# Kernel tuning notes

Measured on AMD Instinct MI355X. Metric: run time of the kernel, lower is better.

## Reference

```python
import jax, jax.numpy as jnp
import numpy as np

N, E = 50000, 800000
NFEAT, NHID, NCLASS = 512, 256, 64
RRELU_SLOPE = (1.0 / 8.0 + 1.0 / 3.0) / 2.0  # nn.RReLU eval-mode negative slope


def spmm(row, col, val, X):
    # sparse adj (COO: row, col, val) @ dense X -> [N, F]
    return jax.ops.segment_sum(X[col] * val[:, None], row, num_segments=N)


def setup_inputs() -> dict:
    key = jax.random.key(0)
    ks = jax.random.split(key, 12)
    x = jax.random.normal(ks[0], (N, NFEAT), dtype=jnp.float32)
    edge_row = jnp.sort(jax.random.randint(ks[1], (E,), 0, N))
    edge_col = jax.random.randint(ks[2], (E,), 0, N)
    # normalized-ish positive adjacency values
    edge_val = jax.random.uniform(ks[3], (E,), dtype=jnp.float32) / 16.0
    def glorot(k, fi, fo):
        s = 1.0 / np.sqrt(fi)
        return jax.random.normal(k, (fi, fo), dtype=jnp.float32) * s
    w1 = glorot(ks[4], NFEAT, NHID)
    b1 = jax.random.normal(ks[5], (NHID,), dtype=jnp.float32) * 0.01
    w2 = glorot(ks[6], NFEAT, NHID)
    b2 = jax.random.normal(ks[7], (NHID,), dtype=jnp.float32) * 0.01
    w3 = glorot(ks[8], NHID, NCLASS)
    b3 = jax.random.normal(ks[9], (NCLASS,), dtype=jnp.float32) * 0.01
    w4 = glorot(ks[10], NFEAT, NCLASS)
    b4 = jax.random.normal(ks[11], (NCLASS,), dtype=jnp.float32) * 0.01
    return {"x": x, "edge_row": edge_row, "edge_col": edge_col, "edge_val": edge_val,
            "w1": w1, "b1": b1, "w2": w2, "b2": b2, "w3": w3, "b3": b3, "w4": w4, "b4": b4}


def reference(x, edge_row, edge_col, edge_val, w1, b1, w2, b2, w3, b3, w4, b4):
    # skip branches (no adj): support = x @ W + b; dropout is identity in eval
    a_skip0 = x @ w2 + b2                                   # [N, NHID]
    a_skip1 = x @ w4 + b4                                   # [N, NCLASS]
    # gc1 with adj
    h1 = spmm(edge_row, edge_col, edge_val, x @ w1) + b1    # [N, NHID]
    v = h1 + a_skip0
    h = jnp.where(v >= 0, v, v * RRELU_SLOPE)               # RReLU (eval mode)
    # gc3 with adj
    out = spmm(edge_row, edge_col, edge_val, h @ w3) + b3 + a_skip1  # [N, NCLASS]
    return (out, w1, w2, w3, w4)
```

## Files before the change

### kernel.cpp

```cpp
#include <hip/hip_runtime.h>

#define N_NODES 50000
#define N_EDGES 800000
#define NFEAT 512
#define NHID 256
#define NCLASS 64
#define NCOMB 576
#define NPAD 640
#define NSKIP 320
#define RRELU_SLOPE 0.2291666666666667f

typedef __attribute__((ext_vector_type(8))) short bf16x8;
typedef __attribute__((ext_vector_type(4))) float f32x4;
typedef __attribute__((ext_vector_type(2))) float f32x2;

#define GLOAD_LDS16(g, l)                                                      \
    __builtin_amdgcn_global_load_lds(                                          \
        (const __attribute__((address_space(1))) void*)(g),                    \
        (__attribute__((address_space(3))) void*)(l), 16, 0, 0)

__device__ __forceinline__ unsigned short f2bf(float f) {
    unsigned int x = __float_as_uint(f);
    unsigned int r = (x + 0x7fffu + ((x >> 16) & 1u)) >> 16;
    return (unsigned short)r;
}
__device__ __forceinline__ float bf2f(unsigned short u) {
    return __uint_as_float(((unsigned int)u) << 16);
}
__device__ __forceinline__ float bf_lo(unsigned int u) { return __uint_as_float(u << 16); }
__device__ __forceinline__ float bf_hi(unsigned int u) { return __uint_as_float(u & 0xffff0000u); }
__device__ __forceinline__ unsigned char f2fp8(float v) {
    return (unsigned char)__builtin_amdgcn_cvt_pk_fp8_f32(v, v, 0, false);
}

#define P_BT 327680
#define P_TOT 328320
#define PREP_BLOCKS ((P_TOT + 255) / 256)

__global__ __launch_bounds__(256)
void prep(const float* __restrict__ w1, const float* __restrict__ w2,
          const float* __restrict__ w4, const float* __restrict__ b1,
          const float* __restrict__ b2, const float* __restrict__ b3,
          const float* __restrict__ b4, unsigned short* __restrict__ Bt,
          float* __restrict__ biasb) {
    int i = blockIdx.x * 256 + threadIdx.x;
    if (i >= P_TOT) return;
    if (i < P_BT) {
        int c = i >> 9;
        int k = i & 511;
        float v = 0.f;
        if (c < NHID)            v = w1[k * NHID + c];
        else if (c < 2 * NHID)   v = w2[k * NHID + (c - NHID)];
        else if (c < NCOMB)      v = w4[k * NCLASS + (c - 2 * NHID)];
        Bt[i] = f2bf(v);
    } else {
        int b = i - P_BT;
        float v = 0.f;
        if (b >= NHID && b < 2 * NHID)       v = b1[b - NHID] + b2[b - NHID];
        else if (b >= 2 * NHID && b < NCOMB) v = b3[b - 2 * NHID] + b4[b - 2 * NHID];
        biasb[b] = v;
    }
}

#define GBM 128
#define GBK 64
#define NCB0 5
#define NRP0 392
#define T0 800000
#define T1 850001
#define T2 866385
#define T3 944209
#define TAIL_BLOCKS ((T3 + 255) / 256)

template <int BN, int MODE>
__global__ __launch_bounds__(256, 4)
void gemm_bf16(const void* __restrict__ Araw,
               const unsigned short* __restrict__ Bt,
               const float* __restrict__ bias,
               unsigned char* __restrict__ C8,
               unsigned short* __restrict__ skipb,
               int M, int K, int NC,
               const int* __restrict__ erow, const int* __restrict__ ecol,
               const float* __restrict__ ev, const float* __restrict__ w1f,
               const float* __restrict__ w2f, const float* __restrict__ w3f,
               const float* __restrict__ w4f, uint2* __restrict__ ep,
               int* __restrict__ rp, unsigned short* __restrict__ w3t,
               float* __restrict__ outw) {
    constexpr int CF = BN / 32;
    __shared__ unsigned short As[GBM * GBK];
    __shared__ unsigned short Bs[BN * GBK];
    int row0, col0;
    if (MODE == 0) {
        int b = blockIdx.x;
        if (b >= NRP0 * NCB0) {
            int i = (b - NRP0 * NCB0) * 256 + threadIdx.x;
            if (i < T0) {
                uint2 e;
                e.x = (unsigned)ecol[i];
                e.y = __float_as_uint(ev[i]);
                ep[i] = e;
            } else if (i < T1) {
                int n = i - T0;
                int lo = 0, hi = N_EDGES;
                while (lo < hi) {
                    int mid = (lo + hi) >> 1;
                    if (erow[mid] < n) lo = mid + 1; else hi = mid;
                }
                rp[n] = lo;
            } else if (i < T2) {
                int j = i - T1;
                int c = j >> 8;
                int k = j & 255;
                w3t[j] = f2bf(w3f[k * NCLASS + c]);
            } else if (i < T3) {
                int j = i - T2;
                float4* o4 = (float4*)outw;
                if (j < 32768)        o4[800000 + j] = ((const float4*)w1f)[j];
                else if (j < 65536)   o4[832768 + (j - 32768)] = ((const float4*)w2f)[j - 32768];
                else if (j < 69632)   o4[865536 + (j - 65536)] = ((const float4*)w3f)[j - 65536];
                else                  o4[869632 + (j - 69632)] = ((const float4*)w4f)[j - 69632];
            }
            return;
        }
        int g = b / (8 * NCB0);
        int w = b % (8 * NCB0);
        int r = g * 8 + (w & 7);
        int c = w >> 3;
        if (r * GBM >= M) return;
        row0 = r * GBM;
        col0 = c * BN;
    } else {
        col0 = blockIdx.x * BN;
        row0 = blockIdx.y * GBM;
    }
    const int tid  = threadIdx.x;
    const int lane = tid & 63;
    const int wave = tid >> 6;
    const int wr = (wave >> 1) * 64;
    const int wc = (wave & 1) * (BN / 2);
    const int lm = lane & 15;
    const int l4 = lane >> 4;
    const int sw = lm & 7;

    const int sub  = lane >> 3;
    const int slot = lane & 7;
    const int goct = slot ^ sub;

    f32x4 acc[4][CF] = {};

    for (int k0 = 0; k0 < K; k0 += GBK) {
        if (MODE == 0) {
            const float* Ax = (const float*)Araw;
            float4 fl[8];
            #pragma unroll
            for (int p = 0; p < 4; ++p) {
                int chunk = wave * 4 + p;
                int gr = row0 + chunk * 8 + sub;
                if (gr > M - 1) gr = M - 1;
                const float4* g = (const float4*)(Ax + (size_t)gr * K + k0 + goct * 8);
                fl[2 * p]     = g[0];
                fl[2 * p + 1] = g[1];
            }
            #pragma unroll
            for (int p = 0; p < BN / 32; ++p) {
                int chunk = wave * (BN / 32) + p;
                int rb = col0 + chunk * 8 + sub;
                GLOAD_LDS16(Bt + (size_t)rb * K + k0 + goct * 8, Bs + chunk * 512);
            }
            #pragma unroll
            for (int p = 0; p < 4; ++p) {
                unsigned c0, c1, c2, c3;
                asm("v_cvt_pk_bf16_f32 %0, %1, %2" : "=v"(c0) : "v"(fl[2*p].x),     "v"(fl[2*p].y));
                asm("v_cvt_pk_bf16_f32 %0, %1, %2" : "=v"(c1) : "v"(fl[2*p].z),     "v"(fl[2*p].w));
                asm("v_cvt_pk_bf16_f32 %0, %1, %2" : "=v"(c2) : "v"(fl[2*p+1].x),   "v"(fl[2*p+1].y));
                asm("v_cvt_pk_bf16_f32 %0, %1, %2" : "=v"(c3) : "v"(fl[2*p+1].z),   "v"(fl[2*p+1].w));
                uint4 pk;
                pk.x = c0; pk.y = c1; pk.z = c2; pk.w = c3;
                int chunk = wave * 4 + p;
                *((uint4*)(As + chunk * 512) + lane) = pk;
            }
        } else {
            const unsigned short* A = (const unsigned short*)Araw;
            #pragma unroll
            for (int p = 0; p < 4; ++p) {
                int chunk = wave * 4 + p;
                int gr = row0 + chunk * 8 + sub;
                if (gr > M - 1) gr = M - 1;
                GLOAD_LDS16(A + (size_t)gr * K + k0 + goct * 8, As + chunk * 512);
            }
            #pragma unroll
            for (int p = 0; p < BN / 32; ++p) {
                int chunk = wave * (BN / 32) + p;
                int rb = col0 + chunk * 8 + sub;
                GLOAD_LDS16(Bt + (size_t)rb * K + k0 + goct * 8, Bs + chunk * 512);
            }
        }
        __syncthreads();

        #pragma unroll
        for (int kk8 = 0; kk8 < GBK / 8; kk8 += 4) {
            const int so = ((kk8 + l4) ^ sw) * 8;
            bf16x8 bfr[CF];
            #pragma unroll
            for (int j = 0; j < CF; ++j)
                bfr[j] = *(const bf16x8*)(Bs + (wc + j * 16 + lm) * 64 + so);
            #pragma unroll
            for (int i = 0; i < 4; ++i) {
                bf16x8 af = *(const bf16x8*)(As + (wr + i * 16 + lm) * 64 + so);
                #pragma unroll
                for (int j = 0; j < CF; ++j)
                    acc[i][j] = __builtin_amdgcn_mfma_f32_16x16x32_bf16(af, bfr[j], acc[i][j], 0, 0, 0);
            }
        }
        __syncthreads();
    }

    #pragma unroll
    for (int i = 0; i < 4; ++i) {
        #pragma unroll
        for (int j = 0; j < CF; ++j) {
            int col = col0 + wc + j * 16 + lm;
            float bvv = (MODE == 0) ? bias[col] : 0.f;
            #pragma unroll
            for (int r = 0; r < 4; ++r) {
                int row = row0 + wr + i * 16 + l4 * 4 + r;
                if (row < M) {
                    float v = acc[i][j][r];
                    if (MODE == 0) {
                        if (col < NHID)       C8[(size_t)row * NHID + col] = f2fp8(v);
                        else if (col < NCOMB) skipb[(size_t)row * NSKIP + (col - NHID)] = f2bf(v + bvv);
                    } else {
                        C8[(size_t)row * NC + col] = f2fp8(v);
                    }
                }
            }
        }
    }
}

__global__ __launch_bounds__(256)
void spmm1_rrelu(const int* __restrict__ rp, const uint2* __restrict__ ep,
                 const unsigned char* __restrict__ xw1q,
                 const unsigned short* __restrict__ skipb,
                 unsigned short* __restrict__ hb, int n_nodes) {
    int n = blockIdx.x * 4 + (threadIdx.x >> 6);
    if (n >= n_nodes) return;
    int lane = threadIdx.x & 63;
    int f = lane * 4;
    int lo = rp[n], hi = rp[n + 1];
    float s0 = 0.f, s1 = 0.f, s2 = 0.f, s3 = 0.f;
    int e = lo;
    for (; e + 7 < hi; e += 8) {
        uint2 ed[8];
        unsigned p[8];
        #pragma unroll
        for (int q = 0; q < 8; ++q) ed[q] = ep[e + q];
        #pragma unroll
        for (int q = 0; q < 8; ++q)
            p[q] = *(const unsigned*)(xw1q + (size_t)ed[q].x * NHID + f);
        #pragma unroll
        for (int q = 0; q < 8; ++q) {
            float v = __uint_as_float(ed[q].y);
            f32x2 ab = __builtin_amdgcn_cvt_pk_f32_fp8((int)p[q], false);
            f32x2 cd = __builtin_amdgcn_cvt_pk_f32_fp8((int)p[q], true);
            s0 += v * ab.x;
            s1 += v * ab.y;
            s2 += v * cd.x;
            s3 += v * cd.y;
        }
    }
    for (; e < hi; ++e) {
        uint2 ee = ep[e];
        float v = __uint_as_float(ee.y);
        unsigned p = *(const unsigned*)(xw1q + (size_t)ee.x * NHID + f);
        f32x2 ab = __builtin_amdgcn_cvt_pk_f32_fp8((int)p, false);
        f32x2 cd = __builtin_amdgcn_cvt_pk_f32_fp8((int)p, true);
        s0 += v * ab.x;
        s1 += v * ab.y;
        s2 += v * cd.x;
        s3 += v * cd.y;
    }
    ushort4 sk = *(const ushort4*)(skipb + (size_t)n * NSKIP + f);
    float v0 = s0 + bf2f(sk.x), v1 = s1 + bf2f(sk.y);
    float v2 = s2 + bf2f(sk.z), v3 = s3 + bf2f(sk.w);
    v0 = (v0 >= 0.f) ? v0 : v0 * RRELU_SLOPE;
    v1 = (v1 >= 0.f) ? v1 : v1 * RRELU_SLOPE;
    v2 = (v2 >= 0.f) ? v2 : v2 * RRELU_SLOPE;
    v3 = (v3 >= 0.f) ? v3 : v3 * RRELU_SLOPE;
    ushort4 o;
    o.x = f2bf(v0); o.y = f2bf(v1); o.z = f2bf(v2); o.w = f2bf(v3);
    *(ushort4*)(hb + (size_t)n * NHID + f) = o;
}

__global__ __launch_bounds__(256)
void spmm2_out(const int* __restrict__ rp, const uint2* __restrict__ ep,
               const unsigned char* __restrict__ hw3q,
               const unsigned short* __restrict__ skipb,
               float* __restrict__ out, int n_nodes) {
    int n = blockIdx.x * 4 + (threadIdx.x >> 6);
    if (n >= n_nodes) return;
    int lane = threadIdx.x & 63;
    int q = lane >> 4;
    int l = lane & 15;
    int f = l * 4;
    int lo = rp[n], hi = rp[n + 1];
    float s0 = 0.f, s1 = 0.f, s2 = 0.f, s3 = 0.f;
    int e = lo + q;
    for (; e + 4 < hi; e += 8) {
        uint2 ea = ep[e], eb = ep[e + 4];
        unsigned pa = *(const unsigned*)(hw3q + (size_t)ea.x * NCLASS + f);
        unsigned pb = *(const unsigned*)(hw3q + (size_t)eb.x * NCLASS + f);
        float va = __uint_as_float(ea.y), vb = __uint_as_float(eb.y);
        f32x2 a0 = __builtin_amdgcn_cvt_pk_f32_fp8((int)pa, false);
        f32x2 a1 = __builtin_amdgcn_cvt_pk_f32_fp8((int)pa, true);
        f32x2 b0 = __builtin_amdgcn_cvt_pk_f32_fp8((int)pb, false);
        f32x2 b1 = __builtin_amdgcn_cvt_pk_f32_fp8((int)pb, true);
        s0 += va * a0.x + vb * b0.x;
        s1 += va * a0.y + vb * b0.y;
        s2 += va * a1.x + vb * b1.x;
        s3 += va * a1.y + vb * b1.y;
    }
    for (; e < hi; e += 4) {
        uint2 ee = ep[e];
        unsigned p = *(const unsigned*)(hw3q + (size_t)ee.x * NCLASS + f);
        float v = __uint_as_float(ee.y);
        f32x2 ab = __builtin_amdgcn_cvt_pk_f32_fp8((int)p, false);
        f32x2 cd = __builtin_amdgcn_cvt_pk_f32_fp8((int)p, true);
        s0 += v * ab.x;
        s1 += v * ab.y;
        s2 += v * cd.x;
        s3 += v * cd.y;
    }
    s0 += __shfl_xor(s0, 16); s0 += __shfl_xor(s0, 32);
    s1 += __shfl_xor(s1, 16); s1 += __shfl_xor(s1, 32);
    s2 += __shfl_xor(s2, 16); s2 += __shfl_xor(s2, 32);
    s3 += __shfl_xor(s3, 16); s3 += __shfl_xor(s3, 32);
    if (q == 0) {
        uint2 sv = *(const uint2*)(skipb + (size_t)n * NSKIP + NHID + f);
        float4 o;
        o.x = s0 + bf_lo(sv.x);
        o.y = s1 + bf_hi(sv.x);
        o.z = s2 + bf_lo(sv.y);
        o.w = s3 + bf_hi(sv.y);
        *(float4*)(out + (size_t)n * NCLASS + f) = o;
    }
}

extern "C" void kernel_launch(void* const* d_in, const int* in_sizes, int n_in,
                              void* d_out, int out_size, void* d_ws, size_t ws_size,
                              hipStream_t stream) {
    const float* x    = (const float*)d_in[0];
    const int*   erow = (const int*)d_in[1];
    const int*   ecol = (const int*)d_in[2];
    const float* ev   = (const float*)d_in[3];
    const float* w1   = (const float*)d_in[4];
    const float* b1   = (const float*)d_in[5];
    const float* w2   = (const float*)d_in[6];
    const float* b2   = (const float*)d_in[7];
    const float* w3   = (const float*)d_in[8];
    const float* b3   = (const float*)d_in[9];
    const float* w4   = (const float*)d_in[10];
    const float* b4   = (const float*)d_in[11];
    float* out = (float*)d_out;

    char* ws = (char*)d_ws;
    size_t off = 0;
    auto alloc = [&](size_t bytes) -> void* {
        off = (off + 255) & ~(size_t)255;
        void* p = ws + off;
        off += bytes;
        return p;
    };

    unsigned short* Bt    = (unsigned short*)alloc((size_t)NFEAT * NPAD * 2);
    float*          biasb = (float*)alloc(NPAD * 4);
    unsigned char*  xw1q  = (unsigned char*)alloc((size_t)N_NODES * NHID);
    unsigned short* skipb = (unsigned short*)alloc((size_t)N_NODES * NSKIP * 2);
    unsigned short* hb    = (unsigned short*)alloc((size_t)N_NODES * NHID * 2);
    unsigned short* w3t   = (unsigned short*)alloc((size_t)NHID * NCLASS * 2);
    unsigned char*  hw3q  = (unsigned char*)alloc((size_t)N_NODES * NCLASS);
    int*            rp    = (int*)alloc((size_t)(N_NODES + 1) * 4);
    uint2*          ep    = (uint2*)alloc((size_t)N_EDGES * 8);

    prep<<<PREP_BLOCKS, 256, 0, stream>>>(w1, w2, w4, b1, b2, b3, b4, Bt, biasb);

    gemm_bf16<128, 0><<<NRP0 * NCB0 + TAIL_BLOCKS, 256, 0, stream>>>(
        x, Bt, biasb, xw1q, skipb, N_NODES, NFEAT, NPAD,
        erow, ecol, ev, w1, w2, w3, w4, ep, rp, w3t, out);

    spmm1_rrelu<<<(N_NODES + 3) / 4, 256, 0, stream>>>(rp, ep, xw1q, skipb, hb, N_NODES);

    dim3 g2(NCLASS / 64, (N_NODES + GBM - 1) / GBM);
    gemm_bf16<64, 1><<<g2, 256, 0, stream>>>(hb, w3t, nullptr, hw3q, nullptr,
                                             N_NODES, NHID, NCLASS,
                                             nullptr, nullptr, nullptr, nullptr,
                                             nullptr, nullptr, nullptr, nullptr,
                                             nullptr, nullptr, nullptr);

    spmm2_out<<<(N_NODES + 3) / 4, 256, 0, stream>>>(rp, ep, hw3q, skipb, out, N_NODES);
}
```

Before: 298.7 us.

## Double-buffer LDS tiles in bf16 GEMM to overlap loads with MFMA

Gives the shared A/B tiles in the GEMM kernel two buffers and prefetches the next K-tile while MFMAs run on the current one, with the fp32-to-bf16 conversion of the prefetched A tile placed after the compute. This lets global load latency overlap with matrix math and removes one barrier per K step. In exchange LDS use doubles and the prefetched fp32 registers stay live across the loop, so the launch-bounds occupancy hint drops from 4 to 2 or 3 blocks per SIMD. That costs occupancy.

```diff
diff --git a/kernel.cpp b/kernel.cpp
--- a/kernel.cpp
+++ b/kernel.cpp
@@ -72,8 +72,8 @@
 #define T3 944209
 #define TAIL_BLOCKS ((T3 + 255) / 256)
 
-template <int BN, int MODE>
-__global__ __launch_bounds__(256, 4)
+template <int BN, int MODE, int MINW>
+__global__ __launch_bounds__(256, MINW)
 void gemm_bf16(const void* __restrict__ Araw,
                const unsigned short* __restrict__ Bt,
                const float* __restrict__ bias,
@@ -87,8 +87,8 @@
                int* __restrict__ rp, unsigned short* __restrict__ w3t,
                float* __restrict__ outw) {
     constexpr int CF = BN / 32;
-    __shared__ unsigned short As[GBM * GBK];
-    __shared__ unsigned short Bs[BN * GBK];
+    __shared__ unsigned short As[2][GBM * GBK];
+    __shared__ unsigned short Bs[2][BN * GBK];
     int row0, col0;
     if (MODE == 0) {
         int b = blockIdx.x;
@@ -147,55 +147,61 @@
     const int goct = slot ^ sub;
 
     f32x4 acc[4][CF] = {};
-
-    for (int k0 = 0; k0 < K; k0 += GBK) {
+    float4 fl[8];
+
+    auto stage_issue = [&](int k0, int buf) {
         if (MODE == 0) {
             const float* Ax = (const float*)Araw;
-            float4 fl[8];
+            #pragma unroll
+            for (int p = 0; p < 4; ++p) {
+                int gr = row0 + (wave * 4 + p) * 8 + sub;
+                if (gr > M - 1) gr = M - 1;
+                const float4* g = (const float4*)(Ax + (size_t)gr * K + k0 + goct * 8);
+                fl[2 * p]     = g[0];
+                fl[2 * p + 1] = g[1];
+            }
+        } else {
+            const unsigned short* A = (const unsigned short*)Araw;
             #pragma unroll
             for (int p = 0; p < 4; ++p) {
                 int chunk = wave * 4 + p;
                 int gr = row0 + chunk * 8 + sub;
                 if (gr > M - 1) gr = M - 1;
-                const float4* g = (const float4*)(Ax + (size_t)gr * K + k0 + goct * 8);
-                fl[2 * p]     = g[0];
-                fl[2 * p + 1] = g[1];
-            }
-            #pragma unroll
-            for (int p = 0; p < BN / 32; ++p) {
-                int chunk = wave * (BN / 32) + p;
-                int rb = col0 + chunk * 8 + sub;
-                GLOAD_LDS16(Bt + (size_t)rb * K + k0 + goct * 8, Bs + chunk * 512);
-            }
+                GLOAD_LDS16(A + (size_t)gr * K + k0 + goct * 8, As[buf] + chunk * 512);
+            }
+        }
+        #pragma unroll
+        for (int p = 0; p < BN / 32; ++p) {
+            int chunk = wave * (BN / 32) + p;
+            int rb = col0 + chunk * 8 + sub;
+            GLOAD_LDS16(Bt + (size_t)rb * K + k0 + goct * 8, Bs[buf] + chunk * 512);
+        }
+    };
+    auto stage_finish = [&](int buf) {
+        if (MODE == 0) {
             #pragma unroll
             for (int p = 0; p < 4; ++p) {
                 unsigned c0, c1, c2, c3;
-                asm("v_cvt_pk_bf16_f32 %0, %1, %2" : "=v"(c0) : "v"(fl[2*p].x),     "v"(fl[2*p].y));
-                asm("v_cvt_pk_bf16_f32 %0, %1, %2" : "=v"(c1) : "v"(fl[2*p].z),     "v"(fl[2*p].w));
-                asm("v_cvt_pk_bf16_f32 %0, %1, %2" : "=v"(c2) : "v"(fl[2*p+1].x),   "v"(fl[2*p+1].y));
-                asm("v_cvt_pk_bf16_f32 %0, %1, %2" : "=v"(c3) : "v"(fl[2*p+1].z),   "v"(fl[2*p+1].w));
+                asm("v_cvt_pk_bf16_f32 %0, %1, %2" : "=v"(c0) : "v"(fl[2*p].x),   "v"(fl[2*p].y));
+                asm("v_cvt_pk_bf16_f32 %0, %1, %2" : "=v"(c1) : "v"(fl[2*p].z),   "v"(fl[2*p].w));
+                asm("v_cvt_pk_bf16_f32 %0, %1, %2" : "=v"(c2) : "v"(fl[2*p+1].x), "v"(fl[2*p+1].y));
+                asm("v_cvt_pk_bf16_f32 %0, %1, %2" : "=v"(c3) : "v"(fl[2*p+1].z), "v"(fl[2*p+1].w));
                 uint4 pk;
                 pk.x = c0; pk.y = c1; pk.z = c2; pk.w = c3;
-                int chunk = wave * 4 + p;
-                *((uint4*)(As + chunk * 512) + lane) = pk;
-            }
-        } else {
-            const unsigned short* A = (const unsigned short*)Araw;
-            #pragma unroll
-            for (int p = 0; p < 4; ++p) {
-                int chunk = wave * 4 + p;
-                int gr = row0 + chunk * 8 + sub;
-                if (gr > M - 1) gr = M - 1;
-                GLOAD_LDS16(A + (size_t)gr * K + k0 + goct * 8, As + chunk * 512);
-            }
-            #pragma unroll
-            for (int p = 0; p < BN / 32; ++p) {
-                int chunk = wave * (BN / 32) + p;
-                int rb = col0 + chunk * 8 + sub;
-                GLOAD_LDS16(Bt + (size_t)rb * K + k0 + goct * 8, Bs + chunk * 512);
-            }
-        }
-        __syncthreads();
+                *((uint4*)(As[buf] + (wave * 4 + p) * 512) + lane) = pk;
+            }
+        }
+    };
+
+    stage_issue(0, 0);
+    stage_finish(0);
+    __syncthreads();
+
+    const int nt = K / GBK;
+    int cur = 0;
+    for (int t = 0; t < nt; ++t) {
+        const bool more = (t + 1 < nt);
+        if (more) stage_issue((t + 1) * GBK, cur ^ 1);
 
         #pragma unroll
         for (int kk8 = 0; kk8 < GBK / 8; kk8 += 4) {
@@ -203,16 +209,19 @@
             bf16x8 bfr[CF];
             #pragma unroll
             for (int j = 0; j < CF; ++j)
-                bfr[j] = *(const bf16x8*)(Bs + (wc + j * 16 + lm) * 64 + so);
+                bfr[j] = *(const bf16x8*)(Bs[cur] + (wc + j * 16 + lm) * 64 + so);
             #pragma unroll
             for (int i = 0; i < 4; ++i) {
-                bf16x8 af = *(const bf16x8*)(As + (wr + i * 16 + lm) * 64 + so);
+                bf16x8 af = *(const bf16x8*)(As[cur] + (wr + i * 16 + lm) * 64 + so);
                 #pragma unroll
                 for (int j = 0; j < CF; ++j)
                     acc[i][j] = __builtin_amdgcn_mfma_f32_16x16x32_bf16(af, bfr[j], acc[i][j], 0, 0, 0);
             }
         }
+
+        if (more) stage_finish(cur ^ 1);
         __syncthreads();
+        cur ^= 1;
     }
 
     #pragma unroll
@@ -384,18 +393,18 @@
 
     prep<<<PREP_BLOCKS, 256, 0, stream>>>(w1, w2, w4, b1, b2, b3, b4, Bt, biasb);
 
-    gemm_bf16<128, 0><<<NRP0 * NCB0 + TAIL_BLOCKS, 256, 0, stream>>>(
+    gemm_bf16<128, 0, 2><<<NRP0 * NCB0 + TAIL_BLOCKS, 256, 0, stream>>>(
         x, Bt, biasb, xw1q, skipb, N_NODES, NFEAT, NPAD,
         erow, ecol, ev, w1, w2, w3, w4, ep, rp, w3t, out);
 
     spmm1_rrelu<<<(N_NODES + 3) / 4, 256, 0, stream>>>(rp, ep, xw1q, skipb, hb, N_NODES);
 
     dim3 g2(NCLASS / 64, (N_NODES + GBM - 1) / GBM);
-    gemm_bf16<64, 1><<<g2, 256, 0, stream>>>(hb, w3t, nullptr, hw3q, nullptr,
-                                             N_NODES, NHID, NCLASS,
-                                             nullptr, nullptr, nullptr, nullptr,
-                                             nullptr, nullptr, nullptr, nullptr,
-                                             nullptr, nullptr, nullptr);
+    gemm_bf16<64, 1, 3><<<g2, 256, 0, stream>>>(hb, w3t, nullptr, hw3q, nullptr,
+                                                N_NODES, NHID, NCLASS,
+                                                nullptr, nullptr, nullptr, nullptr,
+                                                nullptr, nullptr, nullptr, nullptr,
+                                                nullptr, nullptr, nullptr);
 
     spmm2_out<<<(N_NODES + 3) / 4, 256, 0, stream>>>(rp, ep, hw3q, skipb, out, N_NODES);
 }
```

Measured after the change: 318.6 us. +6.7%, slower.

## Stage fp32 A tiles via direct global-to-LDS loads and convert at fragment read

Applied to the files above, without the earlier changes.

The first GEMM no longer loads fp32 x into registers and converts to bf16 before writing LDS. It streams raw fp32 tiles straight into a doubled-size LDS buffer with global_load_lds and converts to bf16 when building MFMA fragments. This removes the register round trip and lets loads run asynchronously, at the cost of twice the LDS footprint and repeated conversion per wave, so the occupancy hint drops to 3. Both SpMM kernels also fold their remainder loops into the main unrolled loop using clamped indices and zeroed weights.

```diff
diff --git a/kernel.cpp b/kernel.cpp
--- a/kernel.cpp
+++ b/kernel.cpp
@@ -72,8 +72,8 @@
 #define T3 944209
 #define TAIL_BLOCKS ((T3 + 255) / 256)
 
-template <int BN, int MODE>
-__global__ __launch_bounds__(256, 4)
+template <int BN, int MODE, int MINW>
+__global__ __launch_bounds__(256, MINW)
 void gemm_bf16(const void* __restrict__ Araw,
                const unsigned short* __restrict__ Bt,
                const float* __restrict__ bias,
@@ -87,7 +87,7 @@
                int* __restrict__ rp, unsigned short* __restrict__ w3t,
                float* __restrict__ outw) {
     constexpr int CF = BN / 32;
-    __shared__ unsigned short As[GBM * GBK];
+    __shared__ float AsF[MODE == 0 ? GBM * GBK : GBM * GBK / 2];
     __shared__ unsigned short Bs[BN * GBK];
     int row0, col0;
     if (MODE == 0) {
@@ -146,67 +146,68 @@
     const int slot = lane & 7;
     const int goct = slot ^ sub;
 
+    const int sub4 = lane >> 4;
+    const int h    = lane & 15;
+
     f32x4 acc[4][CF] = {};
+
+    const unsigned short* A16 = (const unsigned short*)AsF;
 
     for (int k0 = 0; k0 < K; k0 += GBK) {
         if (MODE == 0) {
             const float* Ax = (const float*)Araw;
-            float4 fl[8];
+            #pragma unroll
+            for (int p = 0; p < 8; ++p) {
+                int chunk = wave * 8 + p;
+                int lr = chunk * 4 + sub4;
+                int gr = row0 + lr;
+                if (gr > M - 1) gr = M - 1;
+                int gslot = (h >> 1) ^ (lr & 7);
+                GLOAD_LDS16(Ax + (size_t)gr * K + k0 + gslot * 8 + (h & 1) * 4,
+                            AsF + chunk * 256);
+            }
+        } else {
+            const unsigned short* A = (const unsigned short*)Araw;
             #pragma unroll
             for (int p = 0; p < 4; ++p) {
                 int chunk = wave * 4 + p;
                 int gr = row0 + chunk * 8 + sub;
                 if (gr > M - 1) gr = M - 1;
-                const float4* g = (const float4*)(Ax + (size_t)gr * K + k0 + goct * 8);
-                fl[2 * p]     = g[0];
-                fl[2 * p + 1] = g[1];
-            }
-            #pragma unroll
-            for (int p = 0; p < BN / 32; ++p) {
-                int chunk = wave * (BN / 32) + p;
-                int rb = col0 + chunk * 8 + sub;
-                GLOAD_LDS16(Bt + (size_t)rb * K + k0 + goct * 8, Bs + chunk * 512);
-            }
-            #pragma unroll
-            for (int p = 0; p < 4; ++p) {
-                unsigned c0, c1, c2, c3;
-                asm("v_cvt_pk_bf16_f32 %0, %1, %2" : "=v"(c0) : "v"(fl[2*p].x),     "v"(fl[2*p].y));
-                asm("v_cvt_pk_bf16_f32 %0, %1, %2" : "=v"(c1) : "v"(fl[2*p].z),     "v"(fl[2*p].w));
-                asm("v_cvt_pk_bf16_f32 %0, %1, %2" : "=v"(c2) : "v"(fl[2*p+1].x),   "v"(fl[2*p+1].y));
-                asm("v_cvt_pk_bf16_f32 %0, %1, %2" : "=v"(c3) : "v"(fl[2*p+1].z),   "v"(fl[2*p+1].w));
-                uint4 pk;
-                pk.x = c0; pk.y = c1; pk.z = c2; pk.w = c3;
-                int chunk = wave * 4 + p;
-                *((uint4*)(As + chunk * 512) + lane) = pk;
-            }
-        } else {
-            const unsigned short* A = (const unsigned short*)Araw;
-            #pragma unroll
-            for (int p = 0; p < 4; ++p) {
-                int chunk = wave * 4 + p;
-                int gr = row0 + chunk * 8 + sub;
-                if (gr > M - 1) gr = M - 1;
-                GLOAD_LDS16(A + (size_t)gr * K + k0 + goct * 8, As + chunk * 512);
-            }
-            #pragma unroll
-            for (int p = 0; p < BN / 32; ++p) {
-                int chunk = wave * (BN / 32) + p;
-                int rb = col0 + chunk * 8 + sub;
-                GLOAD_LDS16(Bt + (size_t)rb * K + k0 + goct * 8, Bs + chunk * 512);
-            }
+                GLOAD_LDS16(A + (size_t)gr * K + k0 + goct * 8,
+                            (unsigned short*)AsF + chunk * 512);
+            }
+        }
+        #pragma unroll
+        for (int p = 0; p < BN / 32; ++p) {
+            int chunk = wave * (BN / 32) + p;
+            int rb = col0 + chunk * 8 + sub;
+            GLOAD_LDS16(Bt + (size_t)rb * K + k0 + goct * 8, Bs + chunk * 512);
         }
         __syncthreads();
 
         #pragma unroll
         for (int kk8 = 0; kk8 < GBK / 8; kk8 += 4) {
-            const int so = ((kk8 + l4) ^ sw) * 8;
+            const int so = (kk8 + l4) ^ sw;
             bf16x8 bfr[CF];
             #pragma unroll
             for (int j = 0; j < CF; ++j)
-                bfr[j] = *(const bf16x8*)(Bs + (wc + j * 16 + lm) * 64 + so);
+                bfr[j] = *(const bf16x8*)(Bs + (wc + j * 16 + lm) * 64 + so * 8);
             #pragma unroll
             for (int i = 0; i < 4; ++i) {
-                bf16x8 af = *(const bf16x8*)(As + (wr + i * 16 + lm) * 64 + so);
+                bf16x8 af;
+                if (MODE == 0) {
+                    const float* ar = AsF + (wr + i * 16 + lm) * 64 + so * 8;
+                    f32x4 a0 = *(const f32x4*)ar;
+                    f32x4 a1 = *(const f32x4*)(ar + 4);
+                    union { unsigned u[4]; bf16x8 v; } up;
+                    asm("v_cvt_pk_bf16_f32 %0, %1, %2" : "=v"(up.u[0]) : "v"(a0.x), "v"(a0.y));
+                    asm("v_cvt_pk_bf16_f32 %0, %1, %2" : "=v"(up.u[1]) : "v"(a0.z), "v"(a0.w));
+                    asm("v_cvt_pk_bf16_f32 %0, %1, %2" : "=v"(up.u[2]) : "v"(a1.x), "v"(a1.y));
+                    asm("v_cvt_pk_bf16_f32 %0, %1, %2" : "=v"(up.u[3]) : "v"(a1.z), "v"(a1.w));
+                    af = up.v;
+                } else {
+                    af = *(const bf16x8*)(A16 + (wr + i * 16 + lm) * 64 + so * 8);
+                }
                 #pragma unroll
                 for (int j = 0; j < CF; ++j)
                     acc[i][j] = __builtin_amdgcn_mfma_f32_16x16x32_bf16(af, bfr[j], acc[i][j], 0, 0, 0);
@@ -249,18 +250,20 @@
     int f = lane * 4;
     int lo = rp[n], hi = rp[n + 1];
     float s0 = 0.f, s1 = 0.f, s2 = 0.f, s3 = 0.f;
-    int e = lo;
-    for (; e + 7 < hi; e += 8) {
+    for (int e = lo; e < hi; e += 8) {
         uint2 ed[8];
         unsigned p[8];
         #pragma unroll
-        for (int q = 0; q < 8; ++q) ed[q] = ep[e + q];
+        for (int q = 0; q < 8; ++q) {
+            int idx = (e + q < hi) ? e + q : hi - 1;
+            ed[q] = ep[idx];
+        }
         #pragma unroll
         for (int q = 0; q < 8; ++q)
             p[q] = *(const unsigned*)(xw1q + (size_t)ed[q].x * NHID + f);
         #pragma unroll
         for (int q = 0; q < 8; ++q) {
-            float v = __uint_as_float(ed[q].y);
+            float v = (e + q < hi) ? __uint_as_float(ed[q].y) : 0.f;
             f32x2 ab = __builtin_amdgcn_cvt_pk_f32_fp8((int)p[q], false);
             f32x2 cd = __builtin_amdgcn_cvt_pk_f32_fp8((int)p[q], true);
             s0 += v * ab.x;
@@ -268,17 +271,6 @@
             s2 += v * cd.x;
             s3 += v * cd.y;
         }
-    }
-    for (; e < hi; ++e) {
-        uint2 ee = ep[e];
-        float v = __uint_as_float(ee.y);
-        unsigned p = *(const unsigned*)(xw1q + (size_t)ee.x * NHID + f);
-        f32x2 ab = __builtin_amdgcn_cvt_pk_f32_fp8((int)p, false);
-        f32x2 cd = __builtin_amdgcn_cvt_pk_f32_fp8((int)p, true);
-        s0 += v * ab.x;
-        s1 += v * ab.y;
-        s2 += v * cd.x;
-        s3 += v * cd.y;
     }
     ushort4 sk = *(const ushort4*)(skipb + (size_t)n * NSKIP + f);
     float v0 = s0 + bf2f(sk.x), v1 = s1 + bf2f(sk.y);
@@ -305,12 +297,13 @@
     int f = l * 4;
     int lo = rp[n], hi = rp[n + 1];
     float s0 = 0.f, s1 = 0.f, s2 = 0.f, s3 = 0.f;
-    int e = lo + q;
-    for (; e + 4 < hi; e += 8) {
-        uint2 ea = ep[e], eb = ep[e + 4];
+    for (int e = lo + q; e < hi; e += 8) {
+        int i1 = (e + 4 < hi) ? e + 4 : hi - 1;
+        uint2 ea = ep[e], eb = ep[i1];
         unsigned pa = *(const unsigned*)(hw3q + (size_t)ea.x * NCLASS + f);
         unsigned pb = *(const unsigned*)(hw3q + (size_t)eb.x * NCLASS + f);
-        float va = __uint_as_float(ea.y), vb = __uint_as_float(eb.y);
+        float va = __uint_as_float(ea.y);
+        float vb = (e + 4 < hi) ? __uint_as_float(eb.y) : 0.f;
         f32x2 a0 = __builtin_amdgcn_cvt_pk_f32_fp8((int)pa, false);
         f32x2 a1 = __builtin_amdgcn_cvt_pk_f32_fp8((int)pa, true);
         f32x2 b0 = __builtin_amdgcn_cvt_pk_f32_fp8((int)pb, false);
@@ -319,17 +312,6 @@
         s1 += va * a0.y + vb * b0.y;
         s2 += va * a1.x + vb * b1.x;
         s3 += va * a1.y + vb * b1.y;
-    }
-    for (; e < hi; e += 4) {
-        uint2 ee = ep[e];
-        unsigned p = *(const unsigned*)(hw3q + (size_t)ee.x * NCLASS + f);
-        float v = __uint_as_float(ee.y);
-        f32x2 ab = __builtin_amdgcn_cvt_pk_f32_fp8((int)p, false);
-        f32x2 cd = __builtin_amdgcn_cvt_pk_f32_fp8((int)p, true);
-        s0 += v * ab.x;
-        s1 += v * ab.y;
-        s2 += v * cd.x;
-        s3 += v * cd.y;
     }
     s0 += __shfl_xor(s0, 16); s0 += __shfl_xor(s0, 32);
     s1 += __shfl_xor(s1, 16); s1 += __shfl_xor(s1, 32);
@@ -384,18 +366,18 @@
 
     prep<<<PREP_BLOCKS, 256, 0, stream>>>(w1, w2, w4, b1, b2, b3, b4, Bt, biasb);
 
-    gemm_bf16<128, 0><<<NRP0 * NCB0 + TAIL_BLOCKS, 256, 0, stream>>>(
+    gemm_bf16<128, 0, 3><<<NRP0 * NCB0 + TAIL_BLOCKS, 256, 0, stream>>>(
         x, Bt, biasb, xw1q, skipb, N_NODES, NFEAT, NPAD,
         erow, ecol, ev, w1, w2, w3, w4, ep, rp, w3t, out);
 
     spmm1_rrelu<<<(N_NODES + 3) / 4, 256, 0, stream>>>(rp, ep, xw1q, skipb, hb, N_NODES);
 
     dim3 g2(NCLASS / 64, (N_NODES + GBM - 1) / GBM);
-    gemm_bf16<64, 1><<<g2, 256, 0, stream>>>(hb, w3t, nullptr, hw3q, nullptr,
-                                             N_NODES, NHID, NCLASS,
-                                             nullptr, nullptr, nullptr, nullptr,
-                                             nullptr, nullptr, nullptr, nullptr,
-                                             nullptr, nullptr, nullptr);
+    gemm_bf16<64, 1, 4><<<g2, 256, 0, stream>>>(hb, w3t, nullptr, hw3q, nullptr,
+                                                N_NODES, NHID, NCLASS,
+                                                nullptr, nullptr, nullptr, nullptr,
+                                                nullptr, nullptr, nullptr, nullptr,
+                                                nullptr, nullptr, nullptr);
 
     spmm2_out<<<(N_NODES + 3) / 4, 256, 0, stream>>>(rp, ep, hw3q, skipb, out, N_NODES);
 }
```

Measured after the change: 301.5 us. Within noise of the previous version (+0.9%).
